# Optimization experiments

Measured on AMD Instinct MI355X. Metric: run time of the kernel, lower is better.

Reference implementation:

```python
import jax, jax.numpy as jnp
import numpy as np
from jax import lax

DIST_THRESH = 180.0
ATT_THRESH = 0.05


def setup_inputs() -> dict:
    key = jax.random.key(0)
    ks = jax.random.split(key, 6)
    B, N, H, W = 16, 512, 25, 25
    F, Fh = H * W, int(H * W * 1.5)  # 625, 937
    x4 = jax.random.normal(ks[0], (B, N, H, W), dtype=jnp.float32) * 0.25
    attention = jax.random.uniform(ks[1], (B, N, 1, 1), dtype=jnp.float32)
    W1 = jax.random.normal(ks[2], (2, F, Fh), dtype=jnp.float32) * (1.0 / np.sqrt(F))
    b1 = jnp.zeros((Fh,), dtype=jnp.float32)
    W2 = jax.random.normal(ks[3], (2, Fh, F), dtype=jnp.float32) * (1.0 / np.sqrt(Fh))
    b2 = jnp.zeros((F,), dtype=jnp.float32)
    return {"x4": x4, "attention": attention, "W1": W1, "b1": b1, "W2": W2, "b2": b2}


def _build_adjacency(X, att):
    """X: [B,N,F] node features, att: [B,N]. Returns thresholded adjacency [B,N,N]."""
    B, N, F = X.shape
    # pairwise L1 distances, row-by-row scan to avoid materializing [B,N,N,F]
    Xs = jnp.swapaxes(X, 0, 1)  # [N,B,F]

    def row(_, xi):  # xi: [B,F]
        d = jnp.sum(jnp.abs(xi[:, None, :] - X), axis=-1)  # [B,N]
        return None, d

    _, D = lax.scan(row, None, Xs)          # [N,B,N]
    D = jnp.swapaxes(D, 0, 1)               # [B,N,N]
    att_d = jnp.abs(att[:, :, None] - att[:, None, :])  # [B,N,N]
    A = ((D <= DIST_THRESH) & (att_d <= ATT_THRESH)).astype(jnp.float32)
    # original only fills i<j and j<i, diagonal stays 0
    A = A * (1.0 - jnp.eye(N, dtype=jnp.float32))
    return A


def _process_graph(A):
    """A + I, then row-normalize by inverse degree (D^-1 (A+I))."""
    N = A.shape[1]
    A = A + jnp.eye(N, dtype=A.dtype)
    deg = jnp.sum(A, axis=-1)               # [B,N]
    dinv = jnp.where(deg > 0, 1.0 / deg, 0.0)
    return dinv[:, :, None] * A


def _cheb_conv(x, L, Wk, b):
    """ChebConv with K=2 over dense normalized graph L: T0=x, T1=Lx."""
    t1 = jnp.einsum('bij,bjf->bif', L, x)
    return jnp.einsum('bnf,fo->bno', x, Wk[0]) + jnp.einsum('bnf,fo->bno', t1, Wk[1]) + b


def reference(x4, attention, W1, b1, W2, b2):
    B, N, H, W = x4.shape
    X = x4.reshape(B, N, H * W)             # [B,N,625] flow_x
    att = attention[:, :, 0, 0]             # [B,N]
    A = _build_adjacency(X, att)
    L = _process_graph(A)
    h = jax.nn.relu(_cheb_conv(X, L, W1, b1))   # [B,N,937]
    out = jax.nn.relu(_cheb_conv(h, L, W2, b2))  # [B,N,625]
    return out
```

## Files before the change

### kernel.cpp

```cpp
#include <hip/hip_runtime.h>
#include <stdint.h>

typedef uint16_t u16;
typedef uint32_t u32;
typedef __attribute__((ext_vector_type(4))) float f32x4;
typedef __attribute__((ext_vector_type(4))) unsigned short us4;
typedef __attribute__((ext_vector_type(8))) unsigned short us8;

#define NB   16
#define NN   512
#define FF   625
#define FH   937
#define ROWS 8192
#define KS1  1280
#define KS2  1920
#define NPX  640
#define NPH  960
#define F4   160
#define GQ   4

using frag_ab = __attribute__((ext_vector_type(8))) short;
using frag_cd = __attribute__((ext_vector_type(4))) float;

__device__ __forceinline__ u16 f32_bf16(float f) {
  union { float f; uint32_t u; } x; x.f = f;
  uint32_t r = x.u + 0x7fffu + ((x.u >> 16) & 1u);
  return (u16)(r >> 16);
}
__device__ __forceinline__ void gload_lds16(const void* g, void* l) {
  __builtin_amdgcn_global_load_lds((__attribute__((address_space(1))) void*)g,
                                   (__attribute__((address_space(3))) void*)l,
                                   16, 0, 0);
}

__global__ __launch_bounds__(256) void prep(
    const float* __restrict__ x4, const float* __restrict__ att,
    const float* __restrict__ W1, const float* __restrict__ W2,
    f32x4* __restrict__ Xpad, u16* __restrict__ Xcat, u16* __restrict__ Xt,
    u16* __restrict__ W1t, u16* __restrict__ W2t,
    u16* __restrict__ order, float* __restrict__ att_s)
{
  const int blk = blockIdx.x;
  const int tid = threadIdx.x;
  if (blk < 4096) {
    const int xcd = blk & 7, loc = blk >> 3;
    const int row0 = xcd * 1024 + loc * 2;
    for (int s = tid; s < 320; s += 256) {
      const int row = row0 + (s >= 160);
      const int k4 = (s >= 160) ? s - 160 : s;
      f32x4 v; us4 o;
      #pragma unroll
      for (int t = 0; t < 4; ++t) {
        const int f = k4 * 4 + t;
        float x = (f < FF) ? x4[(size_t)row * FF + f] : 0.f;
        v[t] = x; o[t] = f32_bf16(x);
      }
      Xpad[(size_t)row * F4 + k4] = v;
      *(us4*)(Xcat + (size_t)row * KS1 + k4 * 4) = o;
    }
  } else if (blk < 9216) {
    __shared__ float tile[32][33];
    const int bb = blk - 4096;
    const int xcd = bb & 7, sub = bb >> 3;
    const int b = xcd * 2 + sub / 320;
    const int t = sub % 320;
    const int ft = t % 20, kt = t / 20;
    const int tx = tid & 31, ty = tid >> 5;
    #pragma unroll
    for (int r = 0; r < 4; ++r) {
      const int node = kt * 32 + ty + r * 8;
      const int f = ft * 32 + tx;
      tile[ty + r * 8][tx] = (f < FF) ? x4[((size_t)b * NN + node) * FF + f] : 0.f;
    }
    __syncthreads();
    #pragma unroll
    for (int r = 0; r < 4; ++r) {
      const int f = ft * 32 + ty + r * 8;
      const int node = kt * 32 + tx;
      Xt[((size_t)b * NPX + f) * 512 + node] = f32_bf16(tile[tx][ty + r * 8]);
    }
  } else if (blk < 10496) {
    __shared__ float tile[32][33];
    const int bb = blk - 9216;
    const int kt = bb % 40, nt = bb / 40;
    const int tx = tid & 31, ty = tid >> 5;
    #pragma unroll
    for (int r = 0; r < 4; ++r) {
      int k = kt * 32 + ty + r * 8;
      int n = nt * 32 + tx;
      float v = 0.f;
      int c = -1, kk = 0;
      if (k < 625) { c = 0; kk = k; }
      else if (k >= 640 && k < 1265) { c = 1; kk = k - 640; }
      if (c >= 0 && n < FH) v = W1[((size_t)c * 625 + kk) * FH + n];
      tile[ty + r * 8][tx] = v;
    }
    __syncthreads();
    #pragma unroll
    for (int r = 0; r < 4; ++r) {
      int n = nt * 32 + ty + r * 8;
      int k = kt * 32 + tx;
      W1t[(size_t)n * KS1 + k] = f32_bf16(tile[tx][ty + r * 8]);
    }
  } else if (blk < 11696) {
    __shared__ float tile[32][33];
    const int bb = blk - 10496;
    const int kt = bb % 60, nt = bb / 60;
    const int tx = tid & 31, ty = tid >> 5;
    #pragma unroll
    for (int r = 0; r < 4; ++r) {
      int k = kt * 32 + ty + r * 8;
      int n = nt * 32 + tx;
      float v = 0.f;
      int c = -1, kk = 0;
      if (k < 937) { c = 0; kk = k; }
      else if (k >= 960 && k < 1897) { c = 1; kk = k - 960; }
      if (c >= 0 && n < FF) v = W2[((size_t)c * 937 + kk) * FF + n];
      tile[ty + r * 8][tx] = v;
    }
    __syncthreads();
    #pragma unroll
    for (int r = 0; r < 4; ++r) {
      int n = nt * 32 + ty + r * 8;
      int k = kt * 32 + tx;
      W2t[(size_t)n * KS2 + k] = f32_bf16(tile[tx][ty + r * 8]);
    }
  } else {
    __shared__ float a_sh[512];
    const int b = blk - 11696;
    a_sh[tid]       = att[b * NN + tid];
    a_sh[tid + 256] = att[b * NN + tid + 256];
    __syncthreads();
    #pragma unroll
    for (int h = 0; h < 2; ++h) {
      const int i = tid + h * 256;
      const float ai = a_sh[i];
      int r = 0;
      for (int j = 0; j < NN; ++j) {
        const float aj = a_sh[j];
        r += (aj < ai) || (aj == ai && j < i);
      }
      order[(size_t)b * NN + r] = (u16)i;
      att_s[(size_t)b * NN + r] = ai;
    }
  }
}

__global__ __launch_bounds__(256) void build_L(
    const f32x4* __restrict__ Xpad,
    const u16* __restrict__ order,
    const float* __restrict__ att_s,
    u16* __restrict__ L)
{
  __shared__ float atts[512];
  __shared__ u16 ords[512];
  __shared__ u16 cand[512];
  __shared__ u16 flag[GQ][512];
  __shared__ int ncand, naccs[GQ];

  const int tid = threadIdx.x;
  const int blk = blockIdx.x;
  const int xcd = blk & 7, sub = blk >> 3;
  const int b = xcd * 2 + (sub >> 7);
  const int p0 = (sub & 127) * GQ;
  const f32x4* Xb4 = Xpad + (size_t)b * NN * F4;

  atts[tid]       = att_s[b * NN + tid];
  atts[tid + 256] = att_s[b * NN + tid + 256];
  ords[tid]       = order[b * NN + tid];
  ords[tid + 256] = order[b * NN + tid + 256];
  {
    u32* fz = (u32*)&flag[0][0];
    #pragma unroll
    for (int s = 0; s < GQ; ++s) fz[tid + s * 256] = 0;
  }
  if (tid == 0) ncand = 0;
  if (tid < GQ) naccs[tid] = 0;
  __syncthreads();

  float av[GQ]; int ig[GQ];
  #pragma unroll
  for (int g = 0; g < GQ; ++g) { av[g] = atts[p0 + g]; ig[g] = ords[p0 + g]; }
  if (tid < GQ) flag[tid][ords[p0 + tid]] = 1;

  {
    const float lo = av[0] - 0.0501f, hi = av[GQ - 1] + 0.0501f;
    const bool q0 = (atts[tid] >= lo) && (atts[tid] <= hi);
    const bool q1 = (atts[tid + 256] >= lo) && (atts[tid + 256] <= hi);
    const unsigned long long m0 = __ballot(q0);
    const unsigned long long m1 = __ballot(q1);
    const int c0 = __popcll(m0);
    const int c1 = __popcll(m1);
    const int lane = tid & 63;
    int base = 0;
    if (lane == 0 && (c0 + c1)) base = atomicAdd(&ncand, c0 + c1);
    base = __shfl(base, 0, 64);
    const unsigned long long below = (1ull << lane) - 1ull;
    if (q0) cand[base + __popcll(m0 & below)] = (u16)tid;
    if (q1) cand[base + c0 + __popcll(m1 & below)] = (u16)(tid + 256);
  }
  __syncthreads();
  const int nc = ncand;

  const int hl = tid & 31;
  const int hw = tid >> 5;

  f32x4 xi[GQ][5];
  #pragma unroll
  for (int g = 0; g < GQ; ++g) {
    const f32x4* Xi = Xb4 + (size_t)ig[g] * F4;
    #pragma unroll
    for (int s = 0; s < 5; ++s) xi[g][s] = Xi[s * 32 + hl];
  }

  for (int c = hw; c < nc; c += 8) {
    const int p = cand[c];
    const int j = ords[p];
    const float aj = atts[p];
    const f32x4* Xj = Xb4 + (size_t)j * F4;
    f32x4 xj[5];
    #pragma unroll
    for (int s = 0; s < 5; ++s) xj[s] = Xj[s * 32 + hl];

    float pd[GQ];
    #pragma unroll
    for (int g = 0; g < GQ; ++g) {
      float p2 = 0.f;
      #pragma unroll
      for (int t = 0; t < 4; ++t) {
        p2 += fabsf(xi[g][0][t] - xj[0][t]) + fabsf(xi[g][1][t] - xj[1][t])
            + fabsf(xi[g][2][t] - xj[2][t]) + fabsf(xi[g][3][t] - xj[3][t])
            + fabsf(xi[g][4][t] - xj[4][t]);
      }
      pd[g] = p2;
    }
    #pragma unroll
    for (int off = 16; off; off >>= 1) {
      #pragma unroll
      for (int g = 0; g < GQ; ++g) pd[g] += __shfl_xor(pd[g], off, 64);
    }
    if (hl == 0) {
      #pragma unroll
      for (int g = 0; g < GQ; ++g) {
        if (pd[g] <= 180.0f && fabsf(av[g] - aj) <= 0.05f && j != ig[g]) {
          flag[g][j] = 1;
          atomicAdd(&naccs[g], 1);
        }
      }
    }
  }
  __syncthreads();

  #pragma unroll
  for (int g = 0; g < GQ; ++g) {
    const u16 dv = f32_bf16(1.0f / (float)(naccs[g] + 1));
    const long row = (long)b * NN + ig[g];
    const u32 lo2 = flag[g][2 * tid]     ? (u32)dv : 0u;
    const u32 hi2 = flag[g][2 * tid + 1] ? (u32)dv : 0u;
    *(u32*)(L + (size_t)row * 512 + 2 * tid) = lo2 | (hi2 << 16);
  }
}

template <int KS, int NTILE, int NREAL, int NSTORE, bool RELU, bool BIAS, bool OUT_BF16>
__device__ __forceinline__ void gemm_core(
    const u16* __restrict__ At,
    const u16* __restrict__ Btt,
    const float* __restrict__ bias, void* __restrict__ C,
    long crow0, int col0, int ldc)
{
  constexpr int NI = NTILE / 32;
  constexpr int BR = NTILE / 32;
  __shared__ __align__(16) u16 Ash[128 * 64];
  __shared__ __align__(16) u16 Bsh[NTILE * 64];

  const int tid  = threadIdx.x;
  const int lane = tid & 63;
  const int wave = tid >> 6;
  const int wm = wave & 1, wn = wave >> 1;
  const int q = lane >> 4, l16 = lane & 15;

  const u16* pa[4]; const u16* pb[BR];
  #pragma unroll
  for (int r = 0; r < 4; ++r) {
    const int ci = r * 256 + tid;
    const int row = ci >> 3, cpos = ci & 7;
    pa[r] = At + (size_t)row * KS + (cpos ^ (row & 7)) * 8;
  }
  #pragma unroll
  for (int r = 0; r < BR; ++r) {
    const int ci = r * 256 + tid;
    const int row = ci >> 3, cpos = ci & 7;
    pb[r] = Btt + (size_t)row * KS + (cpos ^ (row & 7)) * 8;
  }
  const int wbase = (tid & 192) * 8;

  const frag_ab* fA[4][2]; const frag_ab* fB[NI][2];
  #pragma unroll
  for (int mi = 0; mi < 4; ++mi) {
    const int row = wm * 64 + mi * 16 + l16;
    fA[mi][0] = (const frag_ab*)&Ash[row * 64 + ((q    ) ^ (l16 & 7)) * 8];
    fA[mi][1] = (const frag_ab*)&Ash[row * 64 + ((q + 4) ^ (l16 & 7)) * 8];
  }
  #pragma unroll
  for (int ni = 0; ni < NI; ++ni) {
    const int row = wn * (NTILE / 2) + ni * 16 + l16;
    fB[ni][0] = (const frag_ab*)&Bsh[row * 64 + ((q    ) ^ (l16 & 7)) * 8];
    fB[ni][1] = (const frag_ab*)&Bsh[row * 64 + ((q + 4) ^ (l16 & 7)) * 8];
  }

  frag_cd acc[4][NI] = {};

  constexpr int KT = KS / 64;
  for (int kt = 0; kt < KT; ++kt) {
    __syncthreads();
    #pragma unroll
    for (int r = 0; r < 4; ++r) { gload_lds16(pa[r], &Ash[r * 2048 + wbase]); pa[r] += 64; }
    #pragma unroll
    for (int r = 0; r < BR; ++r) { gload_lds16(pb[r], &Bsh[r * 2048 + wbase]); pb[r] += 64; }
    __syncthreads();

    #pragma unroll
    for (int kk = 0; kk < 2; ++kk) {
      frag_ab av[4], bv[NI];
      #pragma unroll
      for (int mi = 0; mi < 4; ++mi) av[mi] = *fA[mi][kk];
      #pragma unroll
      for (int ni = 0; ni < NI; ++ni) bv[ni] = *fB[ni][kk];
      #pragma unroll
      for (int mi = 0; mi < 4; ++mi)
        #pragma unroll
        for (int ni = 0; ni < NI; ++ni)
          acc[mi][ni] = __builtin_amdgcn_mfma_f32_16x16x32_bf16(
              av[mi], bv[ni], acc[mi][ni], 0, 0, 0);
    }
  }

  #pragma unroll
  for (int ni = 0; ni < NI; ++ni) {
    const int col = col0 + wn * (NTILE / 2) + ni * 16 + l16;
    if (col >= NSTORE) continue;
    const bool ok = (col < NREAL);
    float bvv = 0.f;
    if (BIAS) bvv = ok ? bias[col] : 0.f;
    #pragma unroll
    for (int mi = 0; mi < 4; ++mi) {
      #pragma unroll
      for (int r = 0; r < 4; ++r) {
        const long rowg = crow0 + wm * 64 + mi * 16 + q * 4 + r;
        float v = acc[mi][ni][r];
        if (BIAS) v += bvv;
        if (RELU) v = fmaxf(v, 0.f);
        if (!ok) v = 0.f;
        if (OUT_BF16) ((u16*)C)[rowg * (size_t)ldc + col] = f32_bf16(v);
        else          ((float*)C)[rowg * (size_t)ldc + col] = v;
      }
    }
  }
}

template <int KS, int NTILE, int NREAL, int NSTORE, bool RELU, bool BIAS, bool OUT_BF16>
__global__ __launch_bounds__(256) void gemm_dense(
    const u16* __restrict__ A, const u16* __restrict__ Bt,
    const float* __restrict__ bias, void* __restrict__ C, int ldc)
{
  const int x = blockIdx.x;
  const int mt = ((x & 7) << 3) | (x >> 3);
  gemm_core<KS, NTILE, NREAL, NSTORE, RELU, BIAS, OUT_BF16>(
      A + (size_t)mt * 128 * KS, Bt + (size_t)blockIdx.y * NTILE * KS,
      bias, C, (long)mt * 128, blockIdx.y * NTILE, ldc);
}

template <int NP>
__global__ __launch_bounds__(256) void spmm(
    const u16* __restrict__ L, const u16* __restrict__ Bt,
    u16* __restrict__ C, int ldc)
{
  constexpr int TPB = 4 * (NP / 64);
  const int blk = blockIdx.x;
  const int xcd = blk & 7, sub = blk >> 3;
  const int b = xcd * 2 + sub / TPB;
  const int t = sub % TPB;
  const int mt = t & 3, nt = t >> 2;
  gemm_core<512, 64, NP, NP, false, false, true>(
      L + ((size_t)b * 512 + mt * 128) * 512,
      Bt + ((size_t)b * NP + nt * 64) * 512,
      nullptr, C, (long)b * 512 + mt * 128, nt * 64, ldc);
}

__global__ __launch_bounds__(256) void transpose_h(
    const u16* __restrict__ hcat, u16* __restrict__ ht)
{
  __shared__ u16 tile[32][34];
  const int blk = blockIdx.x;
  const int xcd = blk & 7, sub = blk >> 3;
  const int b = xcd * 2 + sub / 480;
  const int t = sub % 480;
  const int kt = t % 16, nt = t / 16;
  const int tid = threadIdx.x;
  const int tx = tid & 31, ty = tid >> 5;
  #pragma unroll
  for (int r = 0; r < 4; ++r) {
    const int node = kt * 32 + ty + r * 8;
    const int n = nt * 32 + tx;
    tile[ty + r * 8][tx] = hcat[((size_t)b * NN + node) * KS2 + n];
  }
  __syncthreads();
  #pragma unroll
  for (int r = 0; r < 4; ++r) {
    const int n = nt * 32 + ty + r * 8;
    const int node = kt * 32 + tx;
    ht[((size_t)b * NPH + n) * 512 + node] = tile[tx][ty + r * 8];
  }
}

extern "C" void kernel_launch(void* const* d_in, const int* in_sizes, int n_in,
                              void* d_out, int out_size, void* d_ws, size_t ws_size,
                              hipStream_t stream) {
  const float* x4  = (const float*)d_in[0];
  const float* att = (const float*)d_in[1];
  const float* W1  = (const float*)d_in[2];
  const float* b1  = (const float*)d_in[3];
  const float* W2  = (const float*)d_in[4];
  const float* b2  = (const float*)d_in[5];
  float* out = (float*)d_out;

  char* ws = (char*)d_ws;
  f32x4* Xpad = (f32x4*)ws;
  u16* ht = (u16*)ws;       ws += (size_t)ROWS * F4 * 16;
  u16* Xcat = (u16*)ws;  ws += (size_t)ROWS * KS1 * 2;
  u16* hcat = (u16*)ws;  ws += (size_t)ROWS * KS2 * 2;
  u16* W1t  = (u16*)ws;  ws += (size_t)1024 * KS1 * 2;
  u16* W2t  = (u16*)ws;  ws += (size_t)640 * KS2 * 2;
  u16* Lm   = (u16*)ws;  ws += (size_t)NB * 512 * 512 * 2;
  u16* Xt   = (u16*)ws;  ws += (size_t)NB * NPX * 512 * 2;
  float* att_s = (float*)ws; ws += (size_t)NB * NN * 4;
  u16* order_  = (u16*)ws;   ws += (size_t)NB * NN * 2;

  prep<<<dim3(11712), 256, 0, stream>>>(x4, att, W1, W2, Xpad, Xcat, Xt,
                                        W1t, W2t, order_, att_s);
  build_L<<<dim3(2048), 256, 0, stream>>>(Xpad, order_, att_s, Lm);
  spmm<NPX><<<dim3(640), 256, 0, stream>>>(Lm, Xt, Xcat + NPX, KS1);
  gemm_dense<KS1, 128, FH, NPH, true, true, true><<<dim3(64, 8), 256, 0, stream>>>(
      Xcat, W1t, b1, (void*)hcat, KS2);
  transpose_h<<<dim3(7680), 256, 0, stream>>>(hcat, ht);
  spmm<NPH><<<dim3(960), 256, 0, stream>>>(Lm, ht, hcat + NPH, KS2);
  gemm_dense<KS2, 64, FF, FF, true, true, false><<<dim3(64, 10), 256, 0, stream>>>(
      hcat, W2t, b2, (void*)out, FF);
}
```

Measured before the change: 238.1 us.

## Fuse x4 pad/convert and transpose passes into one tiled prep stage

Merges the separate Xpad/Xcat row-conversion blocks and the Xt transpose blocks of the prep kernel into one block type. Each block loads a 32-node by 32-feature tile of x4 into double-buffered shared memory, then writes the padded fp32 copy, the bf16 row copy and the bf16 transposed copy from that tile. The goal is to read x4 from global memory once instead of twice and to cut the block count. The attention-sort blocks move to the front of the grid so the long serial ranking loop starts early. Fewer blocks with a five-step inner loop may lower parallelism, and the Xpad/Xcat writes now come from 8-wide tile rows instead of full contiguous rows, so coalescing is weaker.

New measurement: 221.8 us. -6.9%, faster.

```diff
diff --git a/kernel.cpp b/kernel.cpp
--- a/kernel.cpp
+++ b/kernel.cpp
@@ -40,48 +40,97 @@
     u16* __restrict__ W1t, u16* __restrict__ W2t,
     u16* __restrict__ order, float* __restrict__ att_s)
 {
+  __shared__ __align__(16) float smem[2112];
   const int blk = blockIdx.x;
   const int tid = threadIdx.x;
-  if (blk < 4096) {
-    const int xcd = blk & 7, loc = blk >> 3;
-    const int row0 = xcd * 1024 + loc * 2;
-    for (int s = tid; s < 320; s += 256) {
-      const int row = row0 + (s >= 160);
-      const int k4 = (s >= 160) ? s - 160 : s;
-      f32x4 v; us4 o;
-      #pragma unroll
-      for (int t = 0; t < 4; ++t) {
-        const int f = k4 * 4 + t;
-        float x = (f < FF) ? x4[(size_t)row * FF + f] : 0.f;
-        v[t] = x; o[t] = f32_bf16(x);
-      }
-      Xpad[(size_t)row * F4 + k4] = v;
-      *(us4*)(Xcat + (size_t)row * KS1 + k4 * 4) = o;
-    }
-  } else if (blk < 9216) {
-    __shared__ float tile[32][33];
-    const int bb = blk - 4096;
-    const int xcd = bb & 7, sub = bb >> 3;
-    const int b = xcd * 2 + sub / 320;
-    const int t = sub % 320;
-    const int ft = t % 20, kt = t / 20;
+
+  if (blk < 16) {
+    float* a_sh = smem;
+    const int b = blk;
+    a_sh[tid]       = att[b * NN + tid];
+    a_sh[tid + 256] = att[b * NN + tid + 256];
+    __syncthreads();
+    #pragma unroll
+    for (int h = 0; h < 2; ++h) {
+      const int i = tid + h * 256;
+      const float ai = a_sh[i];
+      int r = 0;
+      for (int j = 0; j < NN; ++j) {
+        const float aj = a_sh[j];
+        r += (aj < ai) || (aj == ai && j < i);
+      }
+      order[(size_t)b * NN + r] = (u16)i;
+      att_s[(size_t)b * NN + r] = ai;
+    }
+  } else if (blk < 1040) {
+    float* T = smem;
+    const int idx = blk - 16;
+    const int xcd = idx & 7, sub = idx >> 3;
+    const int b = xcd * 2 + (sub >> 6);
+    const int rr = sub & 63;
+    const int q = rr >> 4;
+    const int nt = rr & 15;
+    const int node0 = nt * 32;
     const int tx = tid & 31, ty = tid >> 5;
-    #pragma unroll
-    for (int r = 0; r < 4; ++r) {
-      const int node = kt * 32 + ty + r * 8;
-      const int f = ft * 32 + tx;
-      tile[ty + r * 8][tx] = (f < FF) ? x4[((size_t)b * NN + node) * FF + f] : 0.f;
-    }
-    __syncthreads();
-    #pragma unroll
-    for (int r = 0; r < 4; ++r) {
-      const int f = ft * 32 + ty + r * 8;
-      const int node = kt * 32 + tx;
-      Xt[((size_t)b * NPX + f) * 512 + node] = f32_bf16(tile[tx][ty + r * 8]);
-    }
-  } else if (blk < 10496) {
-    __shared__ float tile[32][33];
-    const int bb = blk - 9216;
+    const int lrow = tid >> 3, lcol = tid & 7;
+
+    int buf = 0;
+    {
+      const int f0 = q * 160;
+      #pragma unroll
+      for (int r = 0; r < 4; ++r) {
+        const int node = node0 + ty + r * 8;
+        const int f = f0 + tx;
+        T[(ty + r * 8) * 33 + tx] = (f < FF) ? x4[((size_t)b * NN + node) * FF + f] : 0.f;
+      }
+    }
+    __syncthreads();
+
+    for (int c = 0; c < 5; ++c) {
+      const int f0 = q * 160 + c * 32;
+      float vnext[4];
+      const bool has = (c + 1 < 5);
+      if (has) {
+        const int fn = f0 + 32 + tx;
+        #pragma unroll
+        for (int r = 0; r < 4; ++r) {
+          const int node = node0 + ty + r * 8;
+          vnext[r] = (fn < FF) ? x4[((size_t)b * NN + node) * FF + fn] : 0.f;
+        }
+      }
+      {
+        const int node_l = lrow, k4s = lcol;
+        const size_t grow = (size_t)b * NN + node0 + node_l;
+        const int k4 = q * 40 + c * 8 + k4s;
+        f32x4 v; us4 o;
+        #pragma unroll
+        for (int t = 0; t < 4; ++t) {
+          const float x = T[buf * 1056 + node_l * 33 + k4s * 4 + t];
+          v[t] = x; o[t] = f32_bf16(x);
+        }
+        Xpad[grow * F4 + k4] = v;
+        *(us4*)(Xcat + grow * KS1 + k4 * 4) = o;
+      }
+      {
+        const int fl = lrow, nl = lcol;
+        const int f = f0 + fl;
+        us4 ov;
+        #pragma unroll
+        for (int t = 0; t < 4; ++t)
+          ov[t] = f32_bf16(T[buf * 1056 + (nl * 4 + t) * 33 + fl]);
+        *(us4*)(Xt + ((size_t)b * NPX + f) * 512 + node0 + nl * 4) = ov;
+      }
+      if (has) {
+        #pragma unroll
+        for (int r = 0; r < 4; ++r)
+          T[(buf ^ 1) * 1056 + (ty + r * 8) * 33 + tx] = vnext[r];
+        __syncthreads();
+        buf ^= 1;
+      }
+    }
+  } else if (blk < 2320) {
+    float (*tile)[33] = (float(*)[33])smem;
+    const int bb = blk - 1040;
     const int kt = bb % 40, nt = bb / 40;
     const int tx = tid & 31, ty = tid >> 5;
     #pragma unroll
@@ -102,9 +151,9 @@
       int k = kt * 32 + tx;
       W1t[(size_t)n * KS1 + k] = f32_bf16(tile[tx][ty + r * 8]);
     }
-  } else if (blk < 11696) {
-    __shared__ float tile[32][33];
-    const int bb = blk - 10496;
+  } else {
+    float (*tile)[33] = (float(*)[33])smem;
+    const int bb = blk - 2320;
     const int kt = bb % 60, nt = bb / 60;
     const int tx = tid & 31, ty = tid >> 5;
     #pragma unroll
@@ -124,24 +173,6 @@
       int n = nt * 32 + ty + r * 8;
       int k = kt * 32 + tx;
       W2t[(size_t)n * KS2 + k] = f32_bf16(tile[tx][ty + r * 8]);
-    }
-  } else {
-    __shared__ float a_sh[512];
-    const int b = blk - 11696;
-    a_sh[tid]       = att[b * NN + tid];
-    a_sh[tid + 256] = att[b * NN + tid + 256];
-    __syncthreads();
-    #pragma unroll
-    for (int h = 0; h < 2; ++h) {
-      const int i = tid + h * 256;
-      const float ai = a_sh[i];
-      int r = 0;
-      for (int j = 0; j < NN; ++j) {
-        const float aj = a_sh[j];
-        r += (aj < ai) || (aj == ai && j < i);
-      }
-      order[(size_t)b * NN + r] = (u16)i;
-      att_s[(size_t)b * NN + r] = ai;
     }
   }
 }
@@ -436,8 +467,8 @@
   float* att_s = (float*)ws; ws += (size_t)NB * NN * 4;
   u16* order_  = (u16*)ws;   ws += (size_t)NB * NN * 2;
 
-  prep<<<dim3(11712), 256, 0, stream>>>(x4, att, W1, W2, Xpad, Xcat, Xt,
-                                        W1t, W2t, order_, att_s);
+  prep<<<dim3(3520), 256, 0, stream>>>(x4, att, W1, W2, Xpad, Xcat, Xt,
+                                       W1t, W2t, order_, att_s);
   build_L<<<dim3(2048), 256, 0, stream>>>(Xpad, order_, att_s, Lm);
   spmm<NPX><<<dim3(640), 256, 0, stream>>>(Lm, Xt, Xcat + NPX, KS1);
   gemm_dense<KS1, 128, FH, NPH, true, true, true><<<dim3(64, 8), 256, 0, stream>>>(
```

## Reassociate ChebConv as L·(X·W1) and fuse graph build with first GEMM

Applied to the files above, without the earlier changes.

Each ChebConv layer is rewritten from [X, L·X]·[W0;W1] into X·W0 + L·(X·W1). The dense GEMM now produces both X·W0 (fp32) and a transposed bf16 X·W1, and the sparse-style L product adds the first part plus bias and ReLU in its epilogue. This removes the X transpose, the h transpose kernel and the concatenated-K layout. Adjacency construction is co-scheduled in the same launch as the first GEMM, so the two independent stages overlap. The cost is wider GEMM outputs, fp32 intermediate buffers, and the L·(XW) product in layer 1 now running over 937 columns instead of 625.

Result: slower. 278.5 us (+17.0%).

```diff
diff --git a/kernel.cpp b/kernel.cpp
--- a/kernel.cpp
+++ b/kernel.cpp
@@ -5,19 +5,18 @@
 typedef uint32_t u32;
 typedef __attribute__((ext_vector_type(4))) float f32x4;
 typedef __attribute__((ext_vector_type(4))) unsigned short us4;
-typedef __attribute__((ext_vector_type(8))) unsigned short us8;
 
 #define NB   16
 #define NN   512
 #define FF   625
 #define FH   937
 #define ROWS 8192
-#define KS1  1280
-#define KS2  1920
-#define NPX  640
-#define NPH  960
 #define F4   160
 #define GQ   4
+#define KX   640
+#define KH   960
+#define N1   1874
+#define N2   1250
 
 using frag_ab = __attribute__((ext_vector_type(8))) short;
 using frag_cd = __attribute__((ext_vector_type(4))) float;
@@ -36,98 +35,17 @@
 __global__ __launch_bounds__(256) void prep(
     const float* __restrict__ x4, const float* __restrict__ att,
     const float* __restrict__ W1, const float* __restrict__ W2,
-    f32x4* __restrict__ Xpad, u16* __restrict__ Xcat, u16* __restrict__ Xt,
-    u16* __restrict__ W1t, u16* __restrict__ W2t,
+    f32x4* __restrict__ Xpad, u16* __restrict__ Xb,
+    u16* __restrict__ W1ct, u16* __restrict__ W2ct,
     u16* __restrict__ order, float* __restrict__ att_s)
 {
+  __shared__ __align__(16) float smem[1056];
   const int blk = blockIdx.x;
   const int tid = threadIdx.x;
-  if (blk < 4096) {
-    const int xcd = blk & 7, loc = blk >> 3;
-    const int row0 = xcd * 1024 + loc * 2;
-    for (int s = tid; s < 320; s += 256) {
-      const int row = row0 + (s >= 160);
-      const int k4 = (s >= 160) ? s - 160 : s;
-      f32x4 v; us4 o;
-      #pragma unroll
-      for (int t = 0; t < 4; ++t) {
-        const int f = k4 * 4 + t;
-        float x = (f < FF) ? x4[(size_t)row * FF + f] : 0.f;
-        v[t] = x; o[t] = f32_bf16(x);
-      }
-      Xpad[(size_t)row * F4 + k4] = v;
-      *(us4*)(Xcat + (size_t)row * KS1 + k4 * 4) = o;
-    }
-  } else if (blk < 9216) {
-    __shared__ float tile[32][33];
-    const int bb = blk - 4096;
-    const int xcd = bb & 7, sub = bb >> 3;
-    const int b = xcd * 2 + sub / 320;
-    const int t = sub % 320;
-    const int ft = t % 20, kt = t / 20;
-    const int tx = tid & 31, ty = tid >> 5;
-    #pragma unroll
-    for (int r = 0; r < 4; ++r) {
-      const int node = kt * 32 + ty + r * 8;
-      const int f = ft * 32 + tx;
-      tile[ty + r * 8][tx] = (f < FF) ? x4[((size_t)b * NN + node) * FF + f] : 0.f;
-    }
-    __syncthreads();
-    #pragma unroll
-    for (int r = 0; r < 4; ++r) {
-      const int f = ft * 32 + ty + r * 8;
-      const int node = kt * 32 + tx;
-      Xt[((size_t)b * NPX + f) * 512 + node] = f32_bf16(tile[tx][ty + r * 8]);
-    }
-  } else if (blk < 10496) {
-    __shared__ float tile[32][33];
-    const int bb = blk - 9216;
-    const int kt = bb % 40, nt = bb / 40;
-    const int tx = tid & 31, ty = tid >> 5;
-    #pragma unroll
-    for (int r = 0; r < 4; ++r) {
-      int k = kt * 32 + ty + r * 8;
-      int n = nt * 32 + tx;
-      float v = 0.f;
-      int c = -1, kk = 0;
-      if (k < 625) { c = 0; kk = k; }
-      else if (k >= 640 && k < 1265) { c = 1; kk = k - 640; }
-      if (c >= 0 && n < FH) v = W1[((size_t)c * 625 + kk) * FH + n];
-      tile[ty + r * 8][tx] = v;
-    }
-    __syncthreads();
-    #pragma unroll
-    for (int r = 0; r < 4; ++r) {
-      int n = nt * 32 + ty + r * 8;
-      int k = kt * 32 + tx;
-      W1t[(size_t)n * KS1 + k] = f32_bf16(tile[tx][ty + r * 8]);
-    }
-  } else if (blk < 11696) {
-    __shared__ float tile[32][33];
-    const int bb = blk - 10496;
-    const int kt = bb % 60, nt = bb / 60;
-    const int tx = tid & 31, ty = tid >> 5;
-    #pragma unroll
-    for (int r = 0; r < 4; ++r) {
-      int k = kt * 32 + ty + r * 8;
-      int n = nt * 32 + tx;
-      float v = 0.f;
-      int c = -1, kk = 0;
-      if (k < 937) { c = 0; kk = k; }
-      else if (k >= 960 && k < 1897) { c = 1; kk = k - 960; }
-      if (c >= 0 && n < FF) v = W2[((size_t)c * 937 + kk) * FF + n];
-      tile[ty + r * 8][tx] = v;
-    }
-    __syncthreads();
-    #pragma unroll
-    for (int r = 0; r < 4; ++r) {
-      int n = nt * 32 + ty + r * 8;
-      int k = kt * 32 + tx;
-      W2t[(size_t)n * KS2 + k] = f32_bf16(tile[tx][ty + r * 8]);
-    }
-  } else {
-    __shared__ float a_sh[512];
-    const int b = blk - 11696;
+
+  if (blk < 16) {
+    float* a_sh = smem;
+    const int b = blk;
     a_sh[tid]       = att[b * NN + tid];
     a_sh[tid + 256] = att[b * NN + tid + 256];
     __syncthreads();
@@ -143,23 +61,198 @@
       order[(size_t)b * NN + r] = (u16)i;
       att_s[(size_t)b * NN + r] = ai;
     }
-  }
-}
-
-__global__ __launch_bounds__(256) void build_L(
-    const f32x4* __restrict__ Xpad,
-    const u16* __restrict__ order,
-    const float* __restrict__ att_s,
-    u16* __restrict__ L)
-{
-  __shared__ float atts[512];
-  __shared__ u16 ords[512];
-  __shared__ u16 cand[512];
-  __shared__ u16 flag[GQ][512];
-  __shared__ int ncand, naccs[GQ];
-
-  const int tid = threadIdx.x;
-  const int blk = blockIdx.x;
+  } else if (blk < 4112) {
+    const int idx = blk - 16;
+    const int xcd = idx & 7, loc = idx >> 3;
+    const int row0 = xcd * 1024 + loc * 2;
+    for (int s = tid; s < 320; s += 256) {
+      const int row = row0 + (s >= 160);
+      const int k4 = (s >= 160) ? s - 160 : s;
+      f32x4 v; us4 o;
+      #pragma unroll
+      for (int t = 0; t < 4; ++t) {
+        const int f = k4 * 4 + t;
+        float x = (f < FF) ? x4[(size_t)row * FF + f] : 0.f;
+        v[t] = x; o[t] = f32_bf16(x);
+      }
+      Xpad[(size_t)row * F4 + k4] = v;
+      *(us4*)(Xb + (size_t)row * KX + k4 * 4) = o;
+    }
+  } else if (blk < 5312) {
+    float (*tile)[33] = (float(*)[33])smem;
+    const int bb = blk - 4112;
+    const int kt = bb % 20, ntl = bb / 20;
+    const int tx = tid & 31, ty = tid >> 5;
+    #pragma unroll
+    for (int r = 0; r < 4; ++r) {
+      const int k = kt * 32 + ty + r * 8;
+      const int n = ntl * 32 + tx;
+      float v = 0.f;
+      int c = -1, np = 0;
+      if (n < 937) { c = 0; np = n; }
+      else if (n < 1874) { c = 1; np = n - 937; }
+      if (c >= 0 && k < 625) v = W1[((size_t)c * 625 + k) * FH + np];
+      tile[ty + r * 8][tx] = v;
+    }
+    __syncthreads();
+    #pragma unroll
+    for (int r = 0; r < 4; ++r) {
+      const int n = ntl * 32 + ty + r * 8;
+      const int k = kt * 32 + tx;
+      W1ct[(size_t)n * KX + k] = f32_bf16(tile[tx][ty + r * 8]);
+    }
+  } else {
+    float (*tile)[33] = (float(*)[33])smem;
+    const int bb = blk - 5312;
+    const int kt = bb % 30, ntl = bb / 30;
+    const int tx = tid & 31, ty = tid >> 5;
+    #pragma unroll
+    for (int r = 0; r < 4; ++r) {
+      const int k = kt * 32 + ty + r * 8;
+      const int n = ntl * 32 + tx;
+      float v = 0.f;
+      int c = -1, np = 0;
+      if (n < 625) { c = 0; np = n; }
+      else if (n < 1250) { c = 1; np = n - 625; }
+      if (c >= 0 && k < 937) v = W2[((size_t)c * 937 + k) * FF + np];
+      tile[ty + r * 8][tx] = v;
+    }
+    __syncthreads();
+    #pragma unroll
+    for (int r = 0; r < 4; ++r) {
+      const int n = ntl * 32 + ty + r * 8;
+      const int k = kt * 32 + tx;
+      W2ct[(size_t)n * KH + k] = f32_bf16(tile[tx][ty + r * 8]);
+    }
+  }
+}
+
+template <int KS, int NTILE, int MODE, int NA, int NR, int NSTO, int NPB, bool OBF16>
+__device__ __forceinline__ void gemm_core(
+    const u16* __restrict__ At,
+    const u16* __restrict__ Btt,
+    const float* __restrict__ bias, const float* __restrict__ Cadd, int lda,
+    void* __restrict__ C, u16* __restrict__ Ct,
+    long crow0, int col0, int ldc,
+    u16* Ash, u16* Bsh)
+{
+  constexpr int NI = NTILE / 32;
+  constexpr int BR = NTILE / 32;
+
+  const int tid  = threadIdx.x;
+  const int lane = tid & 63;
+  const int wave = tid >> 6;
+  const int wm = wave & 1, wn = wave >> 1;
+  const int q = lane >> 4, l16 = lane & 15;
+
+  const u16* pa[4]; const u16* pb[BR];
+  #pragma unroll
+  for (int r = 0; r < 4; ++r) {
+    const int ci = r * 256 + tid;
+    const int row = ci >> 3, cpos = ci & 7;
+    pa[r] = At + (size_t)row * KS + (cpos ^ (row & 7)) * 8;
+  }
+  #pragma unroll
+  for (int r = 0; r < BR; ++r) {
+    const int ci = r * 256 + tid;
+    const int row = ci >> 3, cpos = ci & 7;
+    pb[r] = Btt + (size_t)row * KS + (cpos ^ (row & 7)) * 8;
+  }
+  const int wbase = (tid & 192) * 8;
+
+  const frag_ab* fA[4][2]; const frag_ab* fB[NI][2];
+  #pragma unroll
+  for (int mi = 0; mi < 4; ++mi) {
+    const int row = wm * 64 + mi * 16 + l16;
+    fA[mi][0] = (const frag_ab*)&Ash[row * 64 + ((q    ) ^ (l16 & 7)) * 8];
+    fA[mi][1] = (const frag_ab*)&Ash[row * 64 + ((q + 4) ^ (l16 & 7)) * 8];
+  }
+  #pragma unroll
+  for (int ni = 0; ni < NI; ++ni) {
+    const int row = wn * (NTILE / 2) + ni * 16 + l16;
+    fB[ni][0] = (const frag_ab*)&Bsh[row * 64 + ((q    ) ^ (l16 & 7)) * 8];
+    fB[ni][1] = (const frag_ab*)&Bsh[row * 64 + ((q + 4) ^ (l16 & 7)) * 8];
+  }
+
+  frag_cd acc[4][NI] = {};
+
+  constexpr int KT = KS / 64;
+  for (int kt = 0; kt < KT; ++kt) {
+    __syncthreads();
+    #pragma unroll
+    for (int r = 0; r < 4; ++r) { gload_lds16(pa[r], &Ash[r * 2048 + wbase]); pa[r] += 64; }
+    #pragma unroll
+    for (int r = 0; r < BR; ++r) { gload_lds16(pb[r], &Bsh[r * 2048 + wbase]); pb[r] += 64; }
+    __syncthreads();
+
+    #pragma unroll
+    for (int kk = 0; kk < 2; ++kk) {
+      frag_ab av[4], bv[NI];
+      #pragma unroll
+      for (int mi = 0; mi < 4; ++mi) av[mi] = *fA[mi][kk];
+      #pragma unroll
+      for (int ni = 0; ni < NI; ++ni) bv[ni] = *fB[ni][kk];
+      #pragma unroll
+      for (int mi = 0; mi < 4; ++mi)
+        #pragma unroll
+        for (int ni = 0; ni < NI; ++ni)
+          acc[mi][ni] = __builtin_amdgcn_mfma_f32_16x16x32_bf16(
+              av[mi], bv[ni], acc[mi][ni], 0, 0, 0);
+    }
+  }
+
+  #pragma unroll
+  for (int ni = 0; ni < NI; ++ni) {
+    const int col = col0 + wn * (NTILE / 2) + ni * 16 + l16;
+    if (col >= NSTO) continue;
+    if (MODE == 0) {
+      const bool wt = (col >= NA);
+      #pragma unroll
+      for (int mi = 0; mi < 4; ++mi) {
+        us4 tv;
+        #pragma unroll
+        for (int r = 0; r < 4; ++r) {
+          const long rowg = crow0 + wm * 64 + mi * 16 + q * 4 + r;
+          const float v = acc[mi][ni][r];
+          if (wt) tv[r] = f32_bf16(v);
+          else    ((float*)C)[rowg * (size_t)ldc + col] = v;
+        }
+        if (wt) {
+          const long bb = crow0 >> 9;
+          const int node = (int)(crow0 & 511) + wm * 64 + mi * 16 + q * 4;
+          *(us4*)(Ct + ((size_t)bb * NPB + (col - NA)) * 512 + node) = tv;
+        }
+      }
+    } else {
+      const bool ok = (col < NR);
+      const float bv = ok ? bias[col] : 0.f;
+      #pragma unroll
+      for (int mi = 0; mi < 4; ++mi) {
+        #pragma unroll
+        for (int r = 0; r < 4; ++r) {
+          const long rowg = crow0 + wm * 64 + mi * 16 + q * 4 + r;
+          float v = 0.f;
+          if (ok) v = fmaxf(acc[mi][ni][r] + Cadd[rowg * (size_t)lda + col] + bv, 0.f);
+          if (OBF16) ((u16*)C)[rowg * (size_t)ldc + col] = f32_bf16(v);
+          else       ((float*)C)[rowg * (size_t)ldc + col] = v;
+        }
+      }
+    }
+  }
+}
+
+__device__ __forceinline__ void build_L_body(
+    u16* smem, const int blk, const int tid,
+    const f32x4* __restrict__ Xpad, const u16* __restrict__ order,
+    const float* __restrict__ att_s, u16* __restrict__ L)
+{
+  float* atts = (float*)smem;
+  u16*  ords  = smem + 1024;
+  u16*  cand  = smem + 1536;
+  u16*  flag  = smem + 2048;
+  int*  ncand = (int*)(smem + 4096);
+  int*  naccs = (int*)(smem + 4098);
+
   const int xcd = blk & 7, sub = blk >> 3;
   const int b = xcd * 2 + (sub >> 7);
   const int p0 = (sub & 127) * GQ;
@@ -170,18 +263,18 @@
   ords[tid]       = order[b * NN + tid];
   ords[tid + 256] = order[b * NN + tid + 256];
   {
-    u32* fz = (u32*)&flag[0][0];
+    u32* fz = (u32*)flag;
     #pragma unroll
     for (int s = 0; s < GQ; ++s) fz[tid + s * 256] = 0;
   }
-  if (tid == 0) ncand = 0;
+  if (tid == 0) *ncand = 0;
   if (tid < GQ) naccs[tid] = 0;
   __syncthreads();
 
   float av[GQ]; int ig[GQ];
   #pragma unroll
   for (int g = 0; g < GQ; ++g) { av[g] = atts[p0 + g]; ig[g] = ords[p0 + g]; }
-  if (tid < GQ) flag[tid][ords[p0 + tid]] = 1;
+  if (tid < GQ) flag[tid * 512 + ords[p0 + tid]] = 1;
 
   {
     const float lo = av[0] - 0.0501f, hi = av[GQ - 1] + 0.0501f;
@@ -193,14 +286,14 @@
     const int c1 = __popcll(m1);
     const int lane = tid & 63;
     int base = 0;
-    if (lane == 0 && (c0 + c1)) base = atomicAdd(&ncand, c0 + c1);
+    if (lane == 0 && (c0 + c1)) base = atomicAdd(ncand, c0 + c1);
     base = __shfl(base, 0, 64);
     const unsigned long long below = (1ull << lane) - 1ull;
     if (q0) cand[base + __popcll(m0 & below)] = (u16)tid;
     if (q1) cand[base + c0 + __popcll(m1 & below)] = (u16)(tid + 256);
   }
   __syncthreads();
-  const int nc = ncand;
+  const int nc = *ncand;
 
   const int hl = tid & 31;
   const int hw = tid >> 5;
@@ -243,7 +336,7 @@
       #pragma unroll
       for (int g = 0; g < GQ; ++g) {
         if (pd[g] <= 180.0f && fabsf(av[g] - aj) <= 0.05f && j != ig[g]) {
-          flag[g][j] = 1;
+          flag[g * 512 + j] = 1;
           atomicAdd(&naccs[g], 1);
         }
       }
@@ -255,162 +348,65 @@
   for (int g = 0; g < GQ; ++g) {
     const u16 dv = f32_bf16(1.0f / (float)(naccs[g] + 1));
     const long row = (long)b * NN + ig[g];
-    const u32 lo2 = flag[g][2 * tid]     ? (u32)dv : 0u;
-    const u32 hi2 = flag[g][2 * tid + 1] ? (u32)dv : 0u;
+    const u32 lo2 = flag[g * 512 + 2 * tid]     ? (u32)dv : 0u;
+    const u32 hi2 = flag[g * 512 + 2 * tid + 1] ? (u32)dv : 0u;
     *(u32*)(L + (size_t)row * 512 + 2 * tid) = lo2 | (hi2 << 16);
   }
 }
 
-template <int KS, int NTILE, int NREAL, int NSTORE, bool RELU, bool BIAS, bool OUT_BF16>
-__device__ __forceinline__ void gemm_core(
-    const u16* __restrict__ At,
-    const u16* __restrict__ Btt,
-    const float* __restrict__ bias, void* __restrict__ C,
-    long crow0, int col0, int ldc)
-{
-  constexpr int NI = NTILE / 32;
-  constexpr int BR = NTILE / 32;
-  __shared__ __align__(16) u16 Ash[128 * 64];
-  __shared__ __align__(16) u16 Bsh[NTILE * 64];
-
-  const int tid  = threadIdx.x;
-  const int lane = tid & 63;
-  const int wave = tid >> 6;
-  const int wm = wave & 1, wn = wave >> 1;
-  const int q = lane >> 4, l16 = lane & 15;
-
-  const u16* pa[4]; const u16* pb[BR];
-  #pragma unroll
-  for (int r = 0; r < 4; ++r) {
-    const int ci = r * 256 + tid;
-    const int row = ci >> 3, cpos = ci & 7;
-    pa[r] = At + (size_t)row * KS + (cpos ^ (row & 7)) * 8;
-  }
-  #pragma unroll
-  for (int r = 0; r < BR; ++r) {
-    const int ci = r * 256 + tid;
-    const int row = ci >> 3, cpos = ci & 7;
-    pb[r] = Btt + (size_t)row * KS + (cpos ^ (row & 7)) * 8;
-  }
-  const int wbase = (tid & 192) * 8;
-
-  const frag_ab* fA[4][2]; const frag_ab* fB[NI][2];
-  #pragma unroll
-  for (int mi = 0; mi < 4; ++mi) {
-    const int row = wm * 64 + mi * 16 + l16;
-    fA[mi][0] = (const frag_ab*)&Ash[row * 64 + ((q    ) ^ (l16 & 7)) * 8];
-    fA[mi][1] = (const frag_ab*)&Ash[row * 64 + ((q + 4) ^ (l16 & 7)) * 8];
-  }
-  #pragma unroll
-  for (int ni = 0; ni < NI; ++ni) {
-    const int row = wn * (NTILE / 2) + ni * 16 + l16;
-    fB[ni][0] = (const frag_ab*)&Bsh[row * 64 + ((q    ) ^ (l16 & 7)) * 8];
-    fB[ni][1] = (const frag_ab*)&Bsh[row * 64 + ((q + 4) ^ (l16 & 7)) * 8];
-  }
-
-  frag_cd acc[4][NI] = {};
-
-  constexpr int KT = KS / 64;
-  for (int kt = 0; kt < KT; ++kt) {
-    __syncthreads();
-    #pragma unroll
-    for (int r = 0; r < 4; ++r) { gload_lds16(pa[r], &Ash[r * 2048 + wbase]); pa[r] += 64; }
-    #pragma unroll
-    for (int r = 0; r < BR; ++r) { gload_lds16(pb[r], &Bsh[r * 2048 + wbase]); pb[r] += 64; }
-    __syncthreads();
-
-    #pragma unroll
-    for (int kk = 0; kk < 2; ++kk) {
-      frag_ab av[4], bv[NI];
-      #pragma unroll
-      for (int mi = 0; mi < 4; ++mi) av[mi] = *fA[mi][kk];
-      #pragma unroll
-      for (int ni = 0; ni < NI; ++ni) bv[ni] = *fB[ni][kk];
-      #pragma unroll
-      for (int mi = 0; mi < 4; ++mi)
-        #pragma unroll
-        for (int ni = 0; ni < NI; ++ni)
-          acc[mi][ni] = __builtin_amdgcn_mfma_f32_16x16x32_bf16(
-              av[mi], bv[ni], acc[mi][ni], 0, 0, 0);
-    }
-  }
-
-  #pragma unroll
-  for (int ni = 0; ni < NI; ++ni) {
-    const int col = col0 + wn * (NTILE / 2) + ni * 16 + l16;
-    if (col >= NSTORE) continue;
-    const bool ok = (col < NREAL);
-    float bvv = 0.f;
-    if (BIAS) bvv = ok ? bias[col] : 0.f;
-    #pragma unroll
-    for (int mi = 0; mi < 4; ++mi) {
-      #pragma unroll
-      for (int r = 0; r < 4; ++r) {
-        const long rowg = crow0 + wm * 64 + mi * 16 + q * 4 + r;
-        float v = acc[mi][ni][r];
-        if (BIAS) v += bvv;
-        if (RELU) v = fmaxf(v, 0.f);
-        if (!ok) v = 0.f;
-        if (OUT_BF16) ((u16*)C)[rowg * (size_t)ldc + col] = f32_bf16(v);
-        else          ((float*)C)[rowg * (size_t)ldc + col] = v;
-      }
-    }
-  }
-}
-
-template <int KS, int NTILE, int NREAL, int NSTORE, bool RELU, bool BIAS, bool OUT_BF16>
-__global__ __launch_bounds__(256) void gemm_dense(
-    const u16* __restrict__ A, const u16* __restrict__ Bt,
-    const float* __restrict__ bias, void* __restrict__ C, int ldc)
-{
+__global__ __launch_bounds__(256) void g1_bl(
+    const u16* __restrict__ Xb, const u16* __restrict__ W1ct,
+    float* __restrict__ G1a, u16* __restrict__ G1bt,
+    const f32x4* __restrict__ Xpad, const u16* __restrict__ order,
+    const float* __restrict__ att_s, u16* __restrict__ L)
+{
+  __shared__ __align__(16) u16 smem[16384];
+  const int blk0 = blockIdx.x;
+  const int g = blk0 / 376, r = blk0 % 376;
+  if (r < 120) {
+    const int idx = g * 120 + r;
+    const int y = idx / 64, x = idx % 64;
+    const int mt = ((x & 7) << 3) | (x >> 3);
+    gemm_core<KX, 128, 0, FH, N1, N1, KH, false>(
+        Xb + (size_t)mt * 128 * KX, W1ct + (size_t)y * 128 * KX,
+        nullptr, nullptr, 0, (void*)G1a, G1bt,
+        (long)mt * 128, y * 128, KH, smem, smem + 8192);
+  } else {
+    build_L_body(smem, g * 256 + (r - 120), threadIdx.x, Xpad, order, att_s, L);
+  }
+}
+
+__global__ __launch_bounds__(256) void g2(
+    const u16* __restrict__ h, const u16* __restrict__ W2ct,
+    float* __restrict__ G2a, u16* __restrict__ G2bt)
+{
+  __shared__ __align__(16) u16 smem[16384];
   const int x = blockIdx.x;
   const int mt = ((x & 7) << 3) | (x >> 3);
-  gemm_core<KS, NTILE, NREAL, NSTORE, RELU, BIAS, OUT_BF16>(
-      A + (size_t)mt * 128 * KS, Bt + (size_t)blockIdx.y * NTILE * KS,
-      bias, C, (long)mt * 128, blockIdx.y * NTILE, ldc);
-}
-
-template <int NP>
-__global__ __launch_bounds__(256) void spmm(
+  gemm_core<KH, 128, 0, FF, N2, N2, KX, false>(
+      h + (size_t)mt * 128 * KH, W2ct + (size_t)blockIdx.y * 128 * KH,
+      nullptr, nullptr, 0, (void*)G2a, G2bt,
+      (long)mt * 128, blockIdx.y * 128, KX, smem, smem + 8192);
+}
+
+template <int NP, int NT, int NR, int NSTO, bool OBF16>
+__global__ __launch_bounds__(256) void spmm_add(
     const u16* __restrict__ L, const u16* __restrict__ Bt,
-    u16* __restrict__ C, int ldc)
-{
-  constexpr int TPB = 4 * (NP / 64);
+    const float* __restrict__ Cadd, int lda,
+    const float* __restrict__ bias, void* __restrict__ C, int ldc)
+{
+  __shared__ __align__(16) u16 smem[(128 + NT) * 64];
+  constexpr int TPB = 4 * (NP / NT);
   const int blk = blockIdx.x;
   const int xcd = blk & 7, sub = blk >> 3;
   const int b = xcd * 2 + sub / TPB;
   const int t = sub % TPB;
   const int mt = t & 3, nt = t >> 2;
-  gemm_core<512, 64, NP, NP, false, false, true>(
+  gemm_core<512, NT, 1, 0, NR, NSTO, 0, OBF16>(
       L + ((size_t)b * 512 + mt * 128) * 512,
-      Bt + ((size_t)b * NP + nt * 64) * 512,
-      nullptr, C, (long)b * 512 + mt * 128, nt * 64, ldc);
-}
-
-__global__ __launch_bounds__(256) void transpose_h(
-    const u16* __restrict__ hcat, u16* __restrict__ ht)
-{
-  __shared__ u16 tile[32][34];
-  const int blk = blockIdx.x;
-  const int xcd = blk & 7, sub = blk >> 3;
-  const int b = xcd * 2 + sub / 480;
-  const int t = sub % 480;
-  const int kt = t % 16, nt = t / 16;
-  const int tid = threadIdx.x;
-  const int tx = tid & 31, ty = tid >> 5;
-  #pragma unroll
-  for (int r = 0; r < 4; ++r) {
-    const int node = kt * 32 + ty + r * 8;
-    const int n = nt * 32 + tx;
-    tile[ty + r * 8][tx] = hcat[((size_t)b * NN + node) * KS2 + n];
-  }
-  __syncthreads();
-  #pragma unroll
-  for (int r = 0; r < 4; ++r) {
-    const int n = nt * 32 + ty + r * 8;
-    const int node = kt * 32 + tx;
-    ht[((size_t)b * NPH + n) * 512 + node] = tile[tx][ty + r * 8];
-  }
+      Bt + ((size_t)b * NP + nt * NT) * 512,
+      bias, Cadd, lda, C, nullptr,
+      (long)b * 512 + mt * 128, nt * NT, ldc, smem, smem + 8192);
 }
 
 extern "C" void kernel_launch(void* const* d_in, const int* in_sizes, int n_in,
@@ -426,24 +422,27 @@
 
   char* ws = (char*)d_ws;
   f32x4* Xpad = (f32x4*)ws;
-  u16* ht = (u16*)ws;       ws += (size_t)ROWS * F4 * 16;
-  u16* Xcat = (u16*)ws;  ws += (size_t)ROWS * KS1 * 2;
-  u16* hcat = (u16*)ws;  ws += (size_t)ROWS * KS2 * 2;
-  u16* W1t  = (u16*)ws;  ws += (size_t)1024 * KS1 * 2;
-  u16* W2t  = (u16*)ws;  ws += (size_t)640 * KS2 * 2;
+  float* G2a  = (float*)ws;
+  ws += (size_t)ROWS * F4 * 16;
+  u16* Xb    = (u16*)ws;
+  u16* G2bt  = (u16*)ws;
+  ws += (size_t)ROWS * KX * 2;
+  u16* W1ct = (u16*)ws;  ws += (size_t)1920 * KX * 2;
+  u16* W2ct = (u16*)ws;  ws += (size_t)1280 * KH * 2;
   u16* Lm   = (u16*)ws;  ws += (size_t)NB * 512 * 512 * 2;
-  u16* Xt   = (u16*)ws;  ws += (size_t)NB * NPX * 512 * 2;
+  float* G1a = (float*)ws; ws += (size_t)ROWS * KH * 4;
+  u16* G1bt = (u16*)ws;  ws += (size_t)NB * KH * 512 * 2;
+  u16* hB   = (u16*)ws;  ws += (size_t)ROWS * KH * 2;
   float* att_s = (float*)ws; ws += (size_t)NB * NN * 4;
   u16* order_  = (u16*)ws;   ws += (size_t)NB * NN * 2;
 
-  prep<<<dim3(11712), 256, 0, stream>>>(x4, att, W1, W2, Xpad, Xcat, Xt,
-                                        W1t, W2t, order_, att_s);
-  build_L<<<dim3(2048), 256, 0, stream>>>(Xpad, order_, att_s, Lm);
-  spmm<NPX><<<dim3(640), 256, 0, stream>>>(Lm, Xt, Xcat + NPX, KS1);
-  gemm_dense<KS1, 128, FH, NPH, true, true, true><<<dim3(64, 8), 256, 0, stream>>>(
-      Xcat, W1t, b1, (void*)hcat, KS2);
-  transpose_h<<<dim3(7680), 256, 0, stream>>>(hcat, ht);
-  spmm<NPH><<<dim3(960), 256, 0, stream>>>(Lm, ht, hcat + NPH, KS2);
-  gemm_dense<KS2, 64, FF, FF, true, true, false><<<dim3(64, 10), 256, 0, stream>>>(
-      hcat, W2t, b2, (void*)out, FF);
-}
+  prep<<<dim3(6512), 256, 0, stream>>>(x4, att, W1, W2, Xpad, Xb, W1ct, W2ct,
+                                       order_, att_s);
+  g1_bl<<<dim3(3008), 256, 0, stream>>>(Xb, W1ct, G1a, G1bt,
+                                        Xpad, order_, att_s, Lm);
+  spmm_add<KH, 96, FH, KH, true><<<dim3(640), 256, 0, stream>>>(
+      Lm, G1bt, G1a, KH, b1, (void*)hB, KH);
+  g2<<<dim3(64, 10), 256, 0, stream>>>(hB, W2ct, G2a, G2bt);
+  spmm_add<KX, 64, FF, FF, false><<<dim3(640), 256, 0, stream>>>(
+      Lm, G2bt, G2a, KX, b2, (void*)out, FF);
+}
```
